# Kernel optimization log

Hardware: AMD Instinct MI355X
Metric: run time of the kernel (lower is better)

The kernel has to match this reference:

```python
import jax, jax.numpy as jnp
import numpy as np

H = 8        # attention heads
TOP_K = 2    # gating top-k
STEPS = 5    # dream_length


def _layernorm(x, w, b, eps=1e-5):
    m = jnp.mean(x, axis=-1, keepdims=True)
    v = jnp.var(x, axis=-1, keepdims=True)
    return (x - m) * jax.lax.rsqrt(v + eps) * w + b


def _mha(x, in_w, in_b, out_w, out_b):
    # torch nn.MultiheadAttention (batch_first, self-attention, eval mode)
    Bx, T, Dm = x.shape
    hd = Dm // H
    qkv = x @ in_w.T + in_b                      # (B, T, 3D)
    q, k, v = jnp.split(qkv, 3, axis=-1)
    sh = lambda t: t.reshape(Bx, T, H, hd).transpose(0, 2, 1, 3)
    q, k, v = sh(q), sh(k), sh(v)
    a = jax.nn.softmax(jnp.einsum('bhqd,bhkd->bhqk', q, k) / np.sqrt(hd).astype(np.float32), axis=-1)
    o = jnp.einsum('bhqk,bhkd->bhqd', a, v).transpose(0, 2, 1, 3).reshape(Bx, T, Dm)
    return o @ out_w.T + out_b


def _triplet_proj(p, x):
    xn = _layernorm(x, p['tln_w'], p['tln_b'])
    h = jax.nn.gelu(xn @ p['tw1'].T + p['tb1'], approximate=False)
    return h @ p['tw2'].T + p['tb2']


def _dream_sequence(p, triplet):
    # triplet: (Bt, 3, D); returns (STEPS, 3, Bt, D)
    Bt, _, Dm = triplet.shape
    seq = [jnp.mean(triplet, axis=1)]
    n_layers = p['an_w'].shape[0]
    for step in range(STEPS):
        st = jnp.stack(seq, axis=1) + p['pos'][:step + 1]   # (Bt, t, D)
        for l in range(n_layers):
            xn = _layernorm(st, p['an_w'][l], p['an_b'][l])
            st = st + _mha(xn, p['in_w'][l], p['in_b'][l], p['ow'][l], p['ob'][l])
            fn = _layernorm(st, p['fn_w'][l], p['fn_b'][l])
            st = st + jax.nn.gelu(fn @ p['w1'][l].T + p['b1'][l], approximate=False) @ p['w2'][l].T + p['b2'][l]
        nxt = _triplet_proj(p, st[:, -1]).reshape(Bt, 3, Dm).mean(axis=1)
        seq.append(nxt)
    embs = jnp.stack(seq[1:], axis=0)                        # (STEPS, Bt, D)
    trip = _triplet_proj(p, embs).reshape(STEPS, Bt, 3, Dm)
    return trip.transpose(0, 2, 1, 3)


def _forward(initial_what, initial_action, initial_result, dream_offsets,
             gw1, gb1, gln_w, gln_b, gw2, gb2,
             pos, an_w, an_b, in_w, in_b, ow, ob, fn_w, fn_b, w1, b1, w2, b2,
             tln_w, tln_b, tw1, tb1, tw2, tb2):
    B, Dm = initial_what.shape
    ND = dream_offsets.shape[0]
    triplet = jnp.stack([initial_what, initial_action, initial_result], axis=1)  # (B, 3, D)
    # --- noisy top-k gating (eval mode: no noise, no dropout) ---
    flat = triplet.reshape(B, 3 * Dm)
    g = jax.nn.gelu(_layernorm(flat @ gw1.T + gb1, gln_w, gln_b), approximate=False)
    logits = g @ gw2.T + gb2                                 # (B, E)
    tv, ti = jax.lax.top_k(logits, TOP_K)
    gates = jax.nn.softmax(tv, axis=-1)
    weights = jnp.zeros_like(logits).at[jnp.arange(B)[:, None], ti].set(gates)
    # --- diversified starts; fold dreams into batch ---
    big = (triplet[None] + dream_offsets[:, None]).reshape(ND * B, 3, Dm)
    ep = dict(pos=pos, an_w=an_w, an_b=an_b, in_w=in_w, in_b=in_b, ow=ow, ob=ob,
              fn_w=fn_w, fn_b=fn_b, w1=w1, b1=b1, w2=w2, b2=b2,
              tln_w=tln_w, tln_b=tln_b, tw1=tw1, tb1=tb1, tw2=tw2, tb2=tb2)
    expert_out = jax.vmap(lambda p: _dream_sequence(p, big))(ep)   # (E, STEPS, 3, ND*B, D)
    E = logits.shape[1]
    expert_out = expert_out.reshape(E, STEPS, 3, ND, B, Dm)
    # weighted combine over experts -> (num_dreams, dream_length, 3, B, D)
    return jnp.einsum('estnbd,be->nstbd', expert_out, weights)


def setup_inputs() -> dict:
    D, E, L, FF, B, ND = 1024, 4, 2, 4096, 512, 3
    ks = iter(jax.random.split(jax.random.key(0), 16))
    nrm = lambda shape, s=1.0: jax.random.normal(next(ks), shape, jnp.float32) * s
    return dict(
        initial_what=nrm((B, D)), initial_action=nrm((B, D)), initial_result=nrm((B, D)),
        dream_offsets=nrm((ND, 3, D), 0.1),
        gw1=nrm((D, 3 * D), (3 * D) ** -0.5), gb1=jnp.zeros((D,)),
        gln_w=jnp.ones((D,)), gln_b=jnp.zeros((D,)),
        gw2=nrm((E, D), D ** -0.5), gb2=jnp.zeros((E,)),
        pos=nrm((E, 10, D)),
        an_w=jnp.ones((E, L, D)), an_b=jnp.zeros((E, L, D)),
        in_w=nrm((E, L, 3 * D, D), D ** -0.5), in_b=jnp.zeros((E, L, 3 * D)),
        ow=nrm((E, L, D, D), D ** -0.5), ob=jnp.zeros((E, L, D)),
        fn_w=jnp.ones((E, L, D)), fn_b=jnp.zeros((E, L, D)),
        w1=nrm((E, L, FF, D), D ** -0.5), b1=jnp.zeros((E, L, FF)),
        w2=nrm((E, L, D, FF), FF ** -0.5), b2=jnp.zeros((E, L, D)),
        tln_w=jnp.ones((E, D)), tln_b=jnp.zeros((E, D)),
        tw1=nrm((E, 2 * D, D), D ** -0.5), tb1=jnp.zeros((E, 2 * D)),
        tw2=nrm((E, 3 * D, 2 * D), (2 * D) ** -0.5), tb2=jnp.zeros((E, 3 * D)),
    )


def reference(initial_what, initial_action, initial_result, dream_offsets,
              gw1, gb1, gln_w, gln_b, gw2, gb2,
              pos, an_w, an_b, in_w, in_b, ow, ob, fn_w, fn_b, w1, b1, w2, b2,
              tln_w, tln_b, tw1, tb1, tw2, tb2):
    return _forward(initial_what, initial_action, initial_result, dream_offsets,
                    gw1, gb1, gln_w, gln_b, gw2, gb2,
                    pos, an_w, an_b, in_w, in_b, ow, ob, fn_w, fn_b, w1, b1, w2, b2,
                    tln_w, tln_b, tw1, tb1, tw2, tb2)
```

## Files before the change

kernel.cpp:

```cpp
#include <hip/hip_runtime.h>
#include <hip/hip_bf16.h>
#include <cstdint>

#define B_  512
#define D_  1024
#define E_  4
#define L_  2
#define FF_ 4096
#define ND_ 3
#define BT_ 1536
#define STEPS_ 5
#define H_ 8
#define PROWS 3584
#define TROWS (PROWS * STEPS_)

typedef __attribute__((ext_vector_type(8))) __bf16 bf16x8;
typedef __attribute__((ext_vector_type(8))) unsigned short u16x8;
typedef __attribute__((ext_vector_type(4))) float f32x4;

static __device__ __forceinline__ float gelu_f(float x) {
    return 0.5f * x * (1.0f + erff(x * 0.70710678118654752f));
}

static __device__ __forceinline__ unsigned short f2bf(float x) {
    unsigned u = __builtin_bit_cast(unsigned, x);
    u = (u + 0x7fff + ((u >> 16) & 1)) >> 16;
    return (unsigned short)u;
}

static __device__ __forceinline__ float bf2f(unsigned short us) {
    unsigned v = (unsigned)us << 16;
    return __builtin_bit_cast(float, v);
}

static __device__ __forceinline__ void gload16(const void* g, void* l) {
    __builtin_amdgcn_global_load_lds(
        (const __attribute__((address_space(1))) unsigned int*)g,
        (__attribute__((address_space(3))) unsigned int*)l, 16, 0, 0);
}

static __device__ __forceinline__ int pad128(int x) { return (x + 127) & ~127; }

template<int ACT, int OUTBF>
__global__ __launch_bounds__(512) void gemm_wf32(
    const unsigned short* __restrict__ A,
    const float* __restrict__ Wb, long wstride, int LDA,
    const float* __restrict__ biasb, long bstride,
    const float* __restrict__ R, long Rld, void* __restrict__ Cout, int N, int K,
    const int* __restrict__ roff, int T)
{
    const long row0 = (long)blockIdx.y * 128;
    if ((int)row0 >= roff[4] * T) return;
    int e = 0;
    while (e < 3 && (int)row0 >= roff[e + 1] * T) ++e;
    const float* W = Wb + (long)e * wstride;
    const float* bias = biasb ? (biasb + (long)e * bstride) : nullptr;

    __shared__ __align__(16) unsigned short As[2 * 128 * 32];
    __shared__ __align__(16) unsigned short Bs[2 * 128 * 32];
    const int t = threadIdx.x;
    const int lane = t & 63;
    const int wid = t >> 6;
    const int wr = wid >> 1;
    const int wc = wid & 1;
    const long col0 = (long)blockIdx.x * 128;
    const int l15 = lane & 15, l4 = lane >> 4;

    f32x4 acc[2][4] = {};

    const unsigned short* Ag = A + (row0 + (t >> 2)) * (long)K + (t & 3) * 8;
    char* AdBase = (char*)As + t * 16;

    const float* Wg = W + (long)(col0 + (t >> 2)) * LDA + (t & 3) * 8;

    const int K32 = K >> 5;
    float4 w0, w1;

    gload16(Ag, AdBase);
    w0 = *(const float4*)(Wg);
    w1 = *(const float4*)(Wg + 4);
    {
        u16x8 p = {f2bf(w0.x), f2bf(w0.y), f2bf(w0.z), f2bf(w0.w),
                   f2bf(w1.x), f2bf(w1.y), f2bf(w1.z), f2bf(w1.w)};
        *(u16x8*)((char*)Bs + t * 16) = p;
    }
    if (K32 > 1) {
        w0 = *(const float4*)(Wg + 32);
        w1 = *(const float4*)(Wg + 36);
    }
    __syncthreads();

    for (int j = 0; j < K32; ++j) {
        const int cur = j & 1;
        const int nxt = cur ^ 1;
        if (j + 1 < K32) {
            gload16(Ag + ((j + 1) << 5), AdBase + nxt * 8192);
            u16x8 p = {f2bf(w0.x), f2bf(w0.y), f2bf(w0.z), f2bf(w0.w),
                       f2bf(w1.x), f2bf(w1.y), f2bf(w1.z), f2bf(w1.w)};
            *(u16x8*)((char*)Bs + nxt * 8192 + t * 16) = p;
        }
        if (j + 2 < K32) {
            const int k2 = (j + 2) << 5;
            w0 = *(const float4*)(Wg + k2);
            w1 = *(const float4*)(Wg + k2 + 4);
        }
        bf16x8 af[2], bf[4];
        #pragma unroll
        for (int m = 0; m < 2; ++m)
            af[m] = *(const bf16x8*)((const char*)As + cur * 8192 + (wr * 32 + m * 16 + l15) * 64 + l4 * 16);
        #pragma unroll
        for (int n = 0; n < 4; ++n)
            bf[n] = *(const bf16x8*)((const char*)Bs + cur * 8192 + (wc * 64 + n * 16 + l15) * 64 + l4 * 16);
        __builtin_amdgcn_s_setprio(1);
        #pragma unroll
        for (int m = 0; m < 2; ++m)
            #pragma unroll
            for (int n = 0; n < 4; ++n)
                acc[m][n] = __builtin_amdgcn_mfma_f32_16x16x32_bf16(af[m], bf[n], acc[m][n], 0, 0, 0);
        __builtin_amdgcn_s_setprio(0);
        __syncthreads();
    }

    #pragma unroll
    for (int n = 0; n < 4; ++n) {
        const long col = col0 + wc * 64 + n * 16 + l15;
        const float bn = bias ? bias[col] : 0.0f;
        #pragma unroll
        for (int m = 0; m < 2; ++m) {
            const long rbase = row0 + wr * 32 + m * 16 + l4 * 4;
            #pragma unroll
            for (int r = 0; r < 4; ++r) {
                float o = acc[m][n][r] + bn;
                if (ACT) o = gelu_f(o);
                const long coff = (rbase + r) * (long)N + col;
                if (R) o += R[(rbase + r) * Rld + col];
                if (OUTBF) ((unsigned short*)Cout)[coff] = f2bf(o);
                else       ((float*)Cout)[coff] = o;
            }
        }
    }
}

__global__ __launch_bounds__(256) void gemm_f32(
    const float* __restrict__ A, const float* __restrict__ W,
    const float* __restrict__ bias, const float* __restrict__ R,
    float* __restrict__ C, int M, int N, int K, int act)
{
    __shared__ float As[16][68];
    __shared__ float Bs[16][68];
    const int tid = threadIdx.x;
    const int tx = tid & 15;
    const int ty = tid >> 4;
    const long row0 = (long)blockIdx.y * 64;
    const long col0 = (long)blockIdx.x * 64;
    const int lr = tid >> 2;
    const int lq = (tid & 3) << 2;
    const float* Ap = A + (row0 + lr) * (long)K + lq;
    const float* Wp = W + (col0 + lr) * (long)K + lq;
    float acc[4][4] = {};
    for (int k0 = 0; k0 < K; k0 += 16) {
        const float4 av = *(const float4*)(Ap + k0);
        const float4 wv = *(const float4*)(Wp + k0);
        __syncthreads();
        As[lq + 0][lr] = av.x; As[lq + 1][lr] = av.y;
        As[lq + 2][lr] = av.z; As[lq + 3][lr] = av.w;
        Bs[lq + 0][lr] = wv.x; Bs[lq + 1][lr] = wv.y;
        Bs[lq + 2][lr] = wv.z; Bs[lq + 3][lr] = wv.w;
        __syncthreads();
        #pragma unroll
        for (int kk = 0; kk < 16; ++kk) {
            const float4 a4 = *(const float4*)&As[kk][ty << 2];
            const float4 b4 = *(const float4*)&Bs[kk][tx << 2];
            const float aa[4] = {a4.x, a4.y, a4.z, a4.w};
            const float bb[4] = {b4.x, b4.y, b4.z, b4.w};
            #pragma unroll
            for (int i = 0; i < 4; ++i)
                #pragma unroll
                for (int j = 0; j < 4; ++j)
                    acc[i][j] = fmaf(aa[i], bb[j], acc[i][j]);
        }
    }
    const float4 bv = *(const float4*)(bias + col0 + (tx << 2));
    const float bb[4] = {bv.x, bv.y, bv.z, bv.w};
    #pragma unroll
    for (int i = 0; i < 4; ++i) {
        const long row = row0 + (ty << 2) + i;
        const long off = row * (long)N + col0 + (tx << 2);
        float o[4];
        #pragma unroll
        for (int j = 0; j < 4; ++j) {
            o[j] = acc[i][j] + bb[j];
            if (act) o[j] = gelu_f(o[j]);
        }
        if (R) {
            const float4 rv = *(const float4*)(R + off);
            o[0] += rv.x; o[1] += rv.y; o[2] += rv.z; o[3] += rv.w;
        }
        *(float4*)(C + off) = make_float4(o[0], o[1], o[2], o[3]);
    }
}

__global__ __launch_bounds__(256) void ln_gate(
    const float* __restrict__ X,
    const float* __restrict__ gamma, const float* __restrict__ beta,
    float* __restrict__ Y)
{
    const long r = blockIdx.x;
    const int tid = threadIdx.x;
    __shared__ float red[8];
    const float4 v = *(const float4*)(X + (r << 10) + (tid << 2));
    float s = v.x + v.y + v.z + v.w;
    #pragma unroll
    for (int off = 32; off; off >>= 1) s += __shfl_xor(s, off);
    if ((tid & 63) == 0) red[tid >> 6] = s;
    __syncthreads();
    const float mean = (red[0] + red[1] + red[2] + red[3]) * (1.0f / 1024.0f);
    const float dx = v.x - mean, dy = v.y - mean, dz = v.z - mean, dw = v.w - mean;
    float s2 = dx * dx + dy * dy + dz * dz + dw * dw;
    #pragma unroll
    for (int off = 32; off; off >>= 1) s2 += __shfl_xor(s2, off);
    if ((tid & 63) == 0) red[4 + (tid >> 6)] = s2;
    __syncthreads();
    const float var = (red[4] + red[5] + red[6] + red[7]) * (1.0f / 1024.0f);
    const float inv = rsqrtf(var + 1e-5f);
    const float4 g = *(const float4*)(gamma + (tid << 2));
    const float4 b = *(const float4*)(beta + (tid << 2));
    float o0 = gelu_f(dx * inv * g.x + b.x);
    float o1 = gelu_f(dy * inv * g.y + b.y);
    float o2 = gelu_f(dz * inv * g.z + b.z);
    float o3 = gelu_f(dw * inv * g.w + b.w);
    *(float4*)(Y + (r << 10) + (tid << 2)) = make_float4(o0, o1, o2, o3);
}

__global__ __launch_bounds__(256) void ln_bt(
    const float* __restrict__ X, long xstride,
    const float* __restrict__ gammaB, const float* __restrict__ betaB, long gstride,
    unsigned short* __restrict__ Y, const int* __restrict__ roff, int T)
{
    const long r = blockIdx.x;
    if ((int)r >= roff[4] * T) return;
    int e = 0;
    while (e < 3 && (int)r >= roff[e + 1] * T) ++e;
    const float* gamma = gammaB + (long)e * gstride;
    const float* beta  = betaB  + (long)e * gstride;

    const int tid = threadIdx.x;
    __shared__ float red[8];
    const float4 v = *(const float4*)(X + r * xstride + (tid << 2));
    float s = v.x + v.y + v.z + v.w;
    #pragma unroll
    for (int off = 32; off; off >>= 1) s += __shfl_xor(s, off);
    if ((tid & 63) == 0) red[tid >> 6] = s;
    __syncthreads();
    const float mean = (red[0] + red[1] + red[2] + red[3]) * (1.0f / 1024.0f);
    const float dx = v.x - mean, dy = v.y - mean, dz = v.z - mean, dw = v.w - mean;
    float s2 = dx * dx + dy * dy + dz * dz + dw * dw;
    #pragma unroll
    for (int off = 32; off; off >>= 1) s2 += __shfl_xor(s2, off);
    if ((tid & 63) == 0) red[4 + (tid >> 6)] = s2;
    __syncthreads();
    const float var = (red[4] + red[5] + red[6] + red[7]) * (1.0f / 1024.0f);
    const float inv = rsqrtf(var + 1e-5f);
    const float4 g = *(const float4*)(gamma + (tid << 2));
    const float4 b = *(const float4*)(beta + (tid << 2));
    const float o0 = dx * inv * g.x + b.x;
    const float o1 = dy * inv * g.y + b.y;
    const float o2 = dz * inv * g.z + b.z;
    const float o3 = dw * inv * g.w + b.w;
    ushort4 o = make_ushort4(f2bf(o0), f2bf(o1), f2bf(o2), f2bf(o3));
    *(ushort4*)(Y + (r << 10) + (tid << 2)) = o;
}

__global__ __launch_bounds__(256) void ln_st_bt(
    const float* __restrict__ seq, const float* __restrict__ posb,
    float* __restrict__ st,
    const float* __restrict__ gammaB, const float* __restrict__ betaB, long gstride,
    unsigned short* __restrict__ Y, const int* __restrict__ roff, int T)
{
    const int r = blockIdx.x;
    const int prow = r / T;
    if (prow >= roff[4]) return;
    int e = 0;
    while (e < 3 && prow >= roff[e + 1]) ++e;
    const int tau = r - prow * T;
    const float* gamma = gammaB + (long)e * gstride;
    const float* beta  = betaB  + (long)e * gstride;

    const int tid = threadIdx.x;
    const int d4 = tid << 2;
    __shared__ float red[8];
    const float4 sv = *(const float4*)(seq + (((long)tau * PROWS + prow) << 10) + d4);
    const float4 pv = *(const float4*)(posb + (((long)e * 10 + tau) << 10) + d4);
    const float4 v = make_float4(sv.x + pv.x, sv.y + pv.y, sv.z + pv.z, sv.w + pv.w);
    *(float4*)(st + ((long)r << 10) + d4) = v;

    float s = v.x + v.y + v.z + v.w;
    #pragma unroll
    for (int off = 32; off; off >>= 1) s += __shfl_xor(s, off);
    if ((tid & 63) == 0) red[tid >> 6] = s;
    __syncthreads();
    const float mean = (red[0] + red[1] + red[2] + red[3]) * (1.0f / 1024.0f);
    const float dx = v.x - mean, dy = v.y - mean, dz = v.z - mean, dw = v.w - mean;
    float s2 = dx * dx + dy * dy + dz * dz + dw * dw;
    #pragma unroll
    for (int off = 32; off; off >>= 1) s2 += __shfl_xor(s2, off);
    if ((tid & 63) == 0) red[4 + (tid >> 6)] = s2;
    __syncthreads();
    const float var = (red[4] + red[5] + red[6] + red[7]) * (1.0f / 1024.0f);
    const float inv = rsqrtf(var + 1e-5f);
    const float4 g = *(const float4*)(gamma + d4);
    const float4 b = *(const float4*)(beta + d4);
    const float o0 = dx * inv * g.x + b.x;
    const float o1 = dy * inv * g.y + b.y;
    const float o2 = dz * inv * g.z + b.z;
    const float o3 = dw * inv * g.w + b.w;
    ushort4 o = make_ushort4(f2bf(o0), f2bf(o1), f2bf(o2), f2bf(o3));
    *(ushort4*)(Y + ((long)r << 10) + d4) = o;
}

template<int TT>
__global__ __launch_bounds__(256) void attn_bt(
    const unsigned short* __restrict__ qkv, unsigned short* __restrict__ o,
    const int* __restrict__ roff)
{
    const int item = (int)(((long)blockIdx.x * 256 + threadIdx.x) >> 6);
    const int lane = threadIdx.x & 63;
    const int tq = item % TT;
    const int h  = (item / TT) & 7;
    const int i  = item / (TT * 8);
    if (i >= roff[4]) return;
    const unsigned short* base = qkv + (long)i * TT * 3072;
    const unsigned short* q = base + (long)tq * 3072 + h * 128;
    const float q0 = bf2f(q[lane]), q1 = bf2f(q[lane + 64]);
    float s[TT];
    const float scale = 0.088388347648318447f;
    #pragma unroll
    for (int tk = 0; tk < TT; ++tk) {
        const unsigned short* k = base + (long)tk * 3072 + 1024 + h * 128;
        float p = q0 * bf2f(k[lane]) + q1 * bf2f(k[lane + 64]);
        #pragma unroll
        for (int off = 32; off; off >>= 1) p += __shfl_xor(p, off);
        s[tk] = p * scale;
    }
    float m = s[0];
    #pragma unroll
    for (int tk = 1; tk < TT; ++tk) m = fmaxf(m, s[tk]);
    float den = 0.f;
    #pragma unroll
    for (int tk = 0; tk < TT; ++tk) { s[tk] = expf(s[tk] - m); den += s[tk]; }
    float o0 = 0.f, o1 = 0.f;
    #pragma unroll
    for (int tk = 0; tk < TT; ++tk) {
        const unsigned short* v = base + (long)tk * 3072 + 2048 + h * 128;
        o0 += s[tk] * bf2f(v[lane]); o1 += s[tk] * bf2f(v[lane + 64]);
    }
    const float id = 1.0f / den;
    unsigned short* op = o + ((long)i * TT + tq) * 1024 + h * 128;
    op[lane] = f2bf(o0 * id); op[lane + 64] = f2bf(o1 * id);
}

template<int TT>
__global__ __launch_bounds__(256) void attn_last(
    const unsigned short* __restrict__ qkv, unsigned short* __restrict__ o,
    const int* __restrict__ roff)
{
    const int item = (int)(((long)blockIdx.x * 256 + threadIdx.x) >> 6);
    const int lane = threadIdx.x & 63;
    const int h  = item & 7;
    const int i  = item >> 3;
    if (i >= roff[4]) return;
    const unsigned short* base = qkv + (long)i * TT * 3072;
    const unsigned short* q = base + (long)(TT - 1) * 3072 + h * 128;
    const float q0 = bf2f(q[lane]), q1 = bf2f(q[lane + 64]);
    float s[TT];
    const float scale = 0.088388347648318447f;
    #pragma unroll
    for (int tk = 0; tk < TT; ++tk) {
        const unsigned short* k = base + (long)tk * 3072 + 1024 + h * 128;
        float p = q0 * bf2f(k[lane]) + q1 * bf2f(k[lane + 64]);
        #pragma unroll
        for (int off = 32; off; off >>= 1) p += __shfl_xor(p, off);
        s[tk] = p * scale;
    }
    float m = s[0];
    #pragma unroll
    for (int tk = 1; tk < TT; ++tk) m = fmaxf(m, s[tk]);
    float den = 0.f;
    #pragma unroll
    for (int tk = 0; tk < TT; ++tk) { s[tk] = expf(s[tk] - m); den += s[tk]; }
    float o0 = 0.f, o1 = 0.f;
    #pragma unroll
    for (int tk = 0; tk < TT; ++tk) {
        const unsigned short* v = base + (long)tk * 3072 + 2048 + h * 128;
        o0 += s[tk] * bf2f(v[lane]); o1 += s[tk] * bf2f(v[lane + 64]);
    }
    const float id = 1.0f / den;
    unsigned short* op = o + (long)i * 1024 + h * 128;
    op[lane] = f2bf(o0 * id); op[lane + 64] = f2bf(o1 * id);
}

__global__ __launch_bounds__(256) void gate_kernel(
    const float* __restrict__ g, const float* __restrict__ gw2,
    const float* __restrict__ gb2, float* __restrict__ wout)
{
    const int b = (int)(((long)blockIdx.x * 256 + threadIdx.x) >> 6);
    const int lane = threadIdx.x & 63;
    float acc[E_] = {};
    const float* row = g + (long)b * 1024;
    for (int d = lane; d < 1024; d += 64) {
        const float x = row[d];
        #pragma unroll
        for (int j = 0; j < E_; ++j) acc[j] += x * gw2[j * 1024 + d];
    }
    #pragma unroll
    for (int j = 0; j < E_; ++j) {
        #pragma unroll
        for (int off = 32; off; off >>= 1) acc[j] += __shfl_xor(acc[j], off);
        acc[j] += gb2[j];
    }
    int i0 = 0; float v0 = acc[0];
    #pragma unroll
    for (int j = 1; j < E_; ++j) if (acc[j] > v0) { v0 = acc[j]; i0 = j; }
    int i1 = -1; float v1 = -1e30f;
    #pragma unroll
    for (int j = 0; j < E_; ++j) if (j != i0 && acc[j] > v1) { v1 = acc[j]; i1 = j; }
    const float p1 = expf(v1 - v0);
    const float den = 1.0f + p1;
    const float g0 = 1.0f / den, g1 = p1 / den;
    if (lane < E_) wout[b * E_ + lane] = (lane == i0) ? g0 : (lane == i1) ? g1 : 0.0f;
}

__global__ __launch_bounds__(64) void build_idx2_kernel(
    const float* __restrict__ wbuf, int* __restrict__ idx,
    int* __restrict__ cnt3, int* __restrict__ roff)
{
    const int lane = threadIdx.x;
    int pads[E_];
    for (int e = 0; e < E_; ++e) {
        int* my = idx + e * BT_;
        int base = 0;
        for (int chunk = 0; chunk < 8; ++chunk) {
            const int b = chunk * 64 + lane;
            const bool sel = wbuf[b * E_ + e] > 0.0f;
            const unsigned long long mask = __ballot(sel);
            const int pos = base + (int)__popcll(mask & ((1ull << lane) - 1ull));
            if (sel) {
                my[3 * pos + 0] = b;
                my[3 * pos + 1] = 512 + b;
                my[3 * pos + 2] = 1024 + b;
            }
            base += (int)__popcll(mask);
        }
        if (lane == 0) cnt3[e] = 3 * base;
        pads[e] = pad128(3 * base);
    }
    if (lane == 0) {
        roff[0] = 0;
        for (int e = 0; e < E_; ++e) roff[e + 1] = roff[e] + pads[e];
    }
}

__global__ __launch_bounds__(256) void seq0_bt(
    const float* __restrict__ w, const float* __restrict__ a,
    const float* __restrict__ rr, const float* __restrict__ doff,
    const int* __restrict__ idx, const int* __restrict__ cnt3,
    const int* __restrict__ roff, float* __restrict__ seq0)
{
    const int prow = blockIdx.x;
    if (prow >= roff[4]) return;
    int e = 0;
    while (e < 3 && prow >= roff[e + 1]) ++e;
    const int j = prow - roff[e];
    const int d4 = threadIdx.x << 2;
    float4 res = make_float4(0.f, 0.f, 0.f, 0.f);
    if (j < cnt3[e]) {
        const int v = idx[e * BT_ + j];
        const int n = v >> 9, b = v & 511;
        const float4 x = *(const float4*)(w + ((long)b << 10) + d4);
        const float4 y = *(const float4*)(a + ((long)b << 10) + d4);
        const float4 z = *(const float4*)(rr + ((long)b << 10) + d4);
        const float4 o0 = *(const float4*)(doff + ((long)(n * 3 + 0) << 10) + d4);
        const float4 o1 = *(const float4*)(doff + ((long)(n * 3 + 1) << 10) + d4);
        const float4 o2 = *(const float4*)(doff + ((long)(n * 3 + 2) << 10) + d4);
        const float c = 1.0f / 3.0f;
        res = make_float4(
            (x.x + y.x + z.x + o0.x + o1.x + o2.x) * c,
            (x.y + y.y + z.y + o0.y + o1.y + o2.y) * c,
            (x.z + y.z + z.z + o0.z + o1.z + o2.z) * c,
            (x.w + y.w + z.w + o0.w + o1.w + o2.w) * c);
    }
    *(float4*)(seq0 + ((long)prow << 10) + d4) = res;
}

__global__ __launch_bounds__(256) void mean3_bt(
    const float* __restrict__ O, float* __restrict__ dst,
    const int* __restrict__ roff)
{
    const int r = blockIdx.x;
    if (r >= roff[4]) return;
    const int d4 = threadIdx.x << 2;
    const float* p = O + (long)r * 3072 + d4;
    const float4 x = *(const float4*)p;
    const float4 y = *(const float4*)(p + 1024);
    const float4 z = *(const float4*)(p + 2048);
    const float c = 1.0f / 3.0f;
    *(float4*)(dst + ((long)r << 10) + d4) = make_float4(
        (x.x + y.x + z.x) * c, (x.y + y.y + z.y) * c,
        (x.z + y.z + z.z) * c, (x.w + y.w + z.w) * c);
}

__global__ __launch_bounds__(256) void scatter_bt(
    const float* __restrict__ O, const float* __restrict__ wbuf,
    const int* __restrict__ idx, const int* __restrict__ cnt3,
    const int* __restrict__ roff, float* __restrict__ out, int e, int s)
{
    const int r = blockIdx.x;
    if (r >= cnt3[e]) return;
    const int prow = roff[e] + r;
    const int v = idx[e * BT_ + r];
    const int n = v >> 9, b = v & 511;
    const float wgt = wbuf[b * E_ + e];
    const int d4 = threadIdx.x << 2;
    const float* orow = O + (long)prow * 3072;
    #pragma unroll
    for (int c = 0; c < 3; ++c) {
        const float4 t = *(const float4*)(orow + c * 1024 + d4);
        float* op = out + (((long)((n * STEPS_ + s) * 3 + c) * B_ + b) << 10) + d4;
        float4 o = *(const float4*)op;
        o.x += wgt * t.x; o.y += wgt * t.y; o.z += wgt * t.z; o.w += wgt * t.w;
        *(float4*)op = o;
    }
}

__global__ __launch_bounds__(256) void build_flat_kernel(
    const float* __restrict__ w, const float* __restrict__ a,
    const float* __restrict__ r, float* __restrict__ flat)
{
    const long e4 = ((long)blockIdx.x * 256 + threadIdx.x) << 2;
    const int b = (int)(e4 / 3072);
    const int cd = (int)(e4 % 3072);
    const int c = cd >> 10, d = cd & 1023;
    const float* src = (c == 0) ? w : (c == 1) ? a : r;
    *(float4*)(flat + e4) = *(const float4*)(src + ((long)b << 10) + d);
}

__global__ __launch_bounds__(256) void zero_kernel(float* __restrict__ p, long n4)
{
    const long stride = (long)gridDim.x * 256;
    for (long i = (long)blockIdx.x * 256 + threadIdx.x; i < n4; i += stride)
        *(float4*)(p + i * 4) = make_float4(0.f, 0.f, 0.f, 0.f);
}


extern "C" void kernel_launch(void* const* d_in, const int* in_sizes, int n_in,
                              void* d_out, int out_size, void* d_ws, size_t ws_size,
                              hipStream_t stream)
{
    const float* iw   = (const float*)d_in[0];
    const float* ia   = (const float*)d_in[1];
    const float* ir   = (const float*)d_in[2];
    const float* doff = (const float*)d_in[3];
    const float* gw1  = (const float*)d_in[4];
    const float* gb1  = (const float*)d_in[5];
    const float* glnw = (const float*)d_in[6];
    const float* glnb = (const float*)d_in[7];
    const float* gw2  = (const float*)d_in[8];
    const float* gb2  = (const float*)d_in[9];
    const float* pos  = (const float*)d_in[10];
    const float* anw  = (const float*)d_in[11];
    const float* anb  = (const float*)d_in[12];
    const float* inw  = (const float*)d_in[13];
    const float* inb  = (const float*)d_in[14];
    const float* oww  = (const float*)d_in[15];
    const float* owb  = (const float*)d_in[16];
    const float* fnw  = (const float*)d_in[17];
    const float* fnb  = (const float*)d_in[18];
    const float* w1   = (const float*)d_in[19];
    const float* b1   = (const float*)d_in[20];
    const float* w2   = (const float*)d_in[21];
    const float* b2   = (const float*)d_in[22];
    const float* tlnw = (const float*)d_in[23];
    const float* tlnb = (const float*)d_in[24];
    const float* tw1  = (const float*)d_in[25];
    const float* tb1  = (const float*)d_in[26];
    const float* tw2  = (const float*)d_in[27];
    const float* tb2  = (const float*)d_in[28];
    float* out = (float*)d_out;

    float* ws    = (float*)d_ws;
    float* wbuf  = ws;
    int*   cnt3  = (int*)(wbuf + 2048);
    int*   roff  = cnt3 + 16;
    int*   idxb  = roff + 16;
    float* flatb = (float*)(idxb + 4 * BT_);
    float* glin  = flatb + (long)B_ * 3072;
    float* seq   = glin + (long)B_ * 1024;
    float* st    = seq + 6L * PROWS * 1024;
    unsigned short* xnB  = (unsigned short*)(st + (long)TROWS * 1024);
    unsigned short* bigB = xnB + (long)TROWS * 1024;
    unsigned short* Fbuf = bigB;
    unsigned short* axB  = xnB;
    float* Obuf = (float*)(bigB + 16777216);
    float* stL  = seq + 5L * PROWS * 1024;
    if (ws_size < 79175712UL * sizeof(float)) return;

    build_flat_kernel<<<B_ * 3, 256, 0, stream>>>(iw, ia, ir, flatb);
    gemm_f32<<<dim3(16, 8), 256, 0, stream>>>(flatb, gw1, gb1, nullptr, glin, B_, 1024, 3072, 0);
    ln_gate<<<B_, 256, 0, stream>>>(glin, glnw, glnb, glin);
    gate_kernel<<<B_ / 4, 256, 0, stream>>>(glin, gw2, gb2, wbuf);
    build_idx2_kernel<<<1, 64, 0, stream>>>(wbuf, idxb, cnt3, roff);

    zero_kernel<<<2048, 256, 0, stream>>>(out, (long)ND_ * STEPS_ * 3 * B_ * 1024 / 4);

    seq0_bt<<<PROWS, 256, 0, stream>>>(iw, ia, ir, doff, idxb, cnt3, roff, seq);

    for (int t = 0; t < STEPS_; ++t) {
        const int T = t + 1;
        const int MT = PROWS * T;

        {
            const int l = 0;
            ln_st_bt<<<MT, 256, 0, stream>>>(seq, pos, st,
                                             anw + l * 1024, anb + l * 1024,
                                             (long)L_ * 1024, xnB, roff, T);
            gemm_wf32<0, 1><<<dim3(24, MT / 128), 512, 0, stream>>>(
                xnB, inw + (long)l * 3072 * 1024, (long)L_ * 3072 * 1024, 1024,
                inb + l * 3072, (long)L_ * 3072, nullptr, 0, bigB, 3072, 1024, roff, T);
            switch (T) {
                case 1: attn_bt<1><<<PROWS * 8 * 1 / 4, 256, 0, stream>>>(bigB, xnB, roff); break;
                case 2: attn_bt<2><<<PROWS * 8 * 2 / 4, 256, 0, stream>>>(bigB, xnB, roff); break;
                case 3: attn_bt<3><<<PROWS * 8 * 3 / 4, 256, 0, stream>>>(bigB, xnB, roff); break;
                case 4: attn_bt<4><<<PROWS * 8 * 4 / 4, 256, 0, stream>>>(bigB, xnB, roff); break;
                case 5: attn_bt<5><<<PROWS * 8 * 5 / 4, 256, 0, stream>>>(bigB, xnB, roff); break;
            }
            gemm_wf32<0, 0><<<dim3(8, MT / 128), 512, 0, stream>>>(
                xnB, oww + (long)l * 1024 * 1024, (long)L_ * 1024 * 1024, 1024,
                owb + l * 1024, (long)L_ * 1024, st, 1024, st, 1024, 1024, roff, T);
            ln_bt<<<MT, 256, 0, stream>>>(st, 1024, fnw + l * 1024, fnb + l * 1024,
                                          (long)L_ * 1024, xnB, roff, T);
            for (int c = 0; c < 2; ++c) {
                gemm_wf32<1, 1><<<dim3(16, MT / 128), 512, 0, stream>>>(
                    xnB, w1 + (long)l * 4096 * 1024 + (long)c * 2048 * 1024,
                    (long)L_ * 4096 * 1024, 1024,
                    b1 + l * 4096 + c * 2048, (long)L_ * 4096, nullptr, 0, bigB, 2048, 1024, roff, T);
                gemm_wf32<0, 0><<<dim3(8, MT / 128), 512, 0, stream>>>(
                    bigB, w2 + (long)l * 1024 * 4096 + (long)c * 2048,
                    (long)L_ * 1024 * 4096, 4096,
                    (c == 0) ? (b2 + l * 1024) : nullptr, (long)L_ * 1024,
                    st, 1024, st, 1024, 2048, roff, T);
            }
        }

        {
            const int l = 1;
            ln_bt<<<MT, 256, 0, stream>>>(st, 1024, anw + l * 1024, anb + l * 1024,
                                          (long)L_ * 1024, xnB, roff, T);
            gemm_wf32<0, 1><<<dim3(24, MT / 128), 512, 0, stream>>>(
                xnB, inw + (long)l * 3072 * 1024, (long)L_ * 3072 * 1024, 1024,
                inb + l * 3072, (long)L_ * 3072, nullptr, 0, bigB, 3072, 1024, roff, T);
            switch (T) {
                case 1: attn_last<1><<<PROWS * 8 / 4, 256, 0, stream>>>(bigB, axB, roff); break;
                case 2: attn_last<2><<<PROWS * 8 / 4, 256, 0, stream>>>(bigB, axB, roff); break;
                case 3: attn_last<3><<<PROWS * 8 / 4, 256, 0, stream>>>(bigB, axB, roff); break;
                case 4: attn_last<4><<<PROWS * 8 / 4, 256, 0, stream>>>(bigB, axB, roff); break;
                case 5: attn_last<5><<<PROWS * 8 / 4, 256, 0, stream>>>(bigB, axB, roff); break;
            }
            gemm_wf32<0, 0><<<dim3(8, PROWS / 128), 512, 0, stream>>>(
                axB, oww + (long)l * 1024 * 1024, (long)L_ * 1024 * 1024, 1024,
                owb + l * 1024, (long)L_ * 1024,
                st + (long)t * 1024, (long)T * 1024, stL, 1024, 1024, roff, 1);
            ln_bt<<<PROWS, 256, 0, stream>>>(stL, 1024, fnw + l * 1024, fnb + l * 1024,
                                             (long)L_ * 1024, xnB, roff, 1);
            for (int c = 0; c < 2; ++c) {
                gemm_wf32<1, 1><<<dim3(16, PROWS / 128), 512, 0, stream>>>(
                    xnB, w1 + (long)l * 4096 * 1024 + (long)c * 2048 * 1024,
                    (long)L_ * 4096 * 1024, 1024,
                    b1 + l * 4096 + c * 2048, (long)L_ * 4096, nullptr, 0, Fbuf, 2048, 1024, roff, 1);
                gemm_wf32<0, 0><<<dim3(8, PROWS / 128), 512, 0, stream>>>(
                    Fbuf, w2 + (long)l * 1024 * 4096 + (long)c * 2048,
                    (long)L_ * 1024 * 4096, 4096,
                    (c == 0) ? (b2 + l * 1024) : nullptr, (long)L_ * 1024,
                    stL, 1024, stL, 1024, 2048, roff, 1);
            }
        }

        ln_bt<<<PROWS, 256, 0, stream>>>(stL, 1024, tlnw, tlnb, 1024, xnB, roff, 1);
        gemm_wf32<1, 1><<<dim3(16, PROWS / 128), 512, 0, stream>>>(
            xnB, tw1, 2048L * 1024, 1024, tb1, 2048, nullptr, 0, Fbuf, 2048, 1024, roff, 1);
        gemm_wf32<0, 0><<<dim3(24, PROWS / 128), 512, 0, stream>>>(
            Fbuf, tw2, 3072L * 2048, 2048, tb2, 3072, nullptr, 0, Obuf, 3072, 2048, roff, 1);
        mean3_bt<<<PROWS, 256, 0, stream>>>(Obuf, seq + (long)(t + 1) * PROWS * 1024, roff);
    }
    for (int s = 0; s < STEPS_; ++s) {
        ln_bt<<<PROWS, 256, 0, stream>>>(seq + (long)(s + 1) * PROWS * 1024, 1024,
                                         tlnw, tlnb, 1024, xnB, roff, 1);
        gemm_wf32<1, 1><<<dim3(16, PROWS / 128), 512, 0, stream>>>(
            xnB, tw1, 2048L * 1024, 1024, tb1, 2048, nullptr, 0, Fbuf, 2048, 1024, roff, 1);
        gemm_wf32<0, 0><<<dim3(24, PROWS / 128), 512, 0, stream>>>(
            Fbuf, tw2, 3072L * 2048, 2048, tb2, 3072, nullptr, 0, Obuf, 3072, 2048, roff, 1);
        for (int e = 0; e < E_; ++e)
            scatter_bt<<<BT_, 256, 0, stream>>>(Obuf, wbuf, idxb, cnt3, roff, out, e, s);
    }
}
```

Baseline: 6.909 ms.

## Pre-convert weights to bf16 once and use bf16-weight GEMM kernel

Adds a pass that converts all expert weight matrices from f32 to bf16 into an extra workspace region. A new GEMM kernel then loads both operands as bf16 via direct-to-LDS loads, replacing per-tile f32 loads and register conversion. This halves weight bandwidth and removes conversion ALU work in every GEMM. In exchange it costs an upfront conversion pass each call and needs a larger workspace; if the workspace is too small it falls back to the old kernel.

```diff
diff --git a/kernel.cpp b/kernel.cpp
--- a/kernel.cpp
+++ b/kernel.cpp
@@ -70,7 +70,6 @@
 
     const unsigned short* Ag = A + (row0 + (t >> 2)) * (long)K + (t & 3) * 8;
     char* AdBase = (char*)As + t * 16;
-
     const float* Wg = W + (long)(col0 + (t >> 2)) * LDA + (t & 3) * 8;
 
     const int K32 = K >> 5;
@@ -103,6 +102,89 @@
             const int k2 = (j + 2) << 5;
             w0 = *(const float4*)(Wg + k2);
             w1 = *(const float4*)(Wg + k2 + 4);
+        }
+        bf16x8 af[2], bf[4];
+        #pragma unroll
+        for (int m = 0; m < 2; ++m)
+            af[m] = *(const bf16x8*)((const char*)As + cur * 8192 + (wr * 32 + m * 16 + l15) * 64 + l4 * 16);
+        #pragma unroll
+        for (int n = 0; n < 4; ++n)
+            bf[n] = *(const bf16x8*)((const char*)Bs + cur * 8192 + (wc * 64 + n * 16 + l15) * 64 + l4 * 16);
+        __builtin_amdgcn_s_setprio(1);
+        #pragma unroll
+        for (int m = 0; m < 2; ++m)
+            #pragma unroll
+            for (int n = 0; n < 4; ++n)
+                acc[m][n] = __builtin_amdgcn_mfma_f32_16x16x32_bf16(af[m], bf[n], acc[m][n], 0, 0, 0);
+        __builtin_amdgcn_s_setprio(0);
+        __syncthreads();
+    }
+
+    #pragma unroll
+    for (int n = 0; n < 4; ++n) {
+        const long col = col0 + wc * 64 + n * 16 + l15;
+        const float bn = bias ? bias[col] : 0.0f;
+        #pragma unroll
+        for (int m = 0; m < 2; ++m) {
+            const long rbase = row0 + wr * 32 + m * 16 + l4 * 4;
+            #pragma unroll
+            for (int r = 0; r < 4; ++r) {
+                float o = acc[m][n][r] + bn;
+                if (ACT) o = gelu_f(o);
+                const long coff = (rbase + r) * (long)N + col;
+                if (R) o += R[(rbase + r) * Rld + col];
+                if (OUTBF) ((unsigned short*)Cout)[coff] = f2bf(o);
+                else       ((float*)Cout)[coff] = o;
+            }
+        }
+    }
+}
+
+template<int ACT, int OUTBF>
+__global__ __launch_bounds__(512) void gemm_bb(
+    const unsigned short* __restrict__ A,
+    const unsigned short* __restrict__ Wb, long wstride, int LDA,
+    const float* __restrict__ biasb, long bstride,
+    const float* __restrict__ R, long Rld, void* __restrict__ Cout, int N, int K,
+    const int* __restrict__ roff, int T)
+{
+    const long row0 = (long)blockIdx.y * 128;
+    if ((int)row0 >= roff[4] * T) return;
+    int e = 0;
+    while (e < 3 && (int)row0 >= roff[e + 1] * T) ++e;
+    const unsigned short* W = Wb + (long)e * wstride;
+    const float* bias = biasb ? (biasb + (long)e * bstride) : nullptr;
+
+    __shared__ __align__(16) unsigned short As[2 * 128 * 32];
+    __shared__ __align__(16) unsigned short Bs[2 * 128 * 32];
+    const int t = threadIdx.x;
+    const int lane = t & 63;
+    const int wid = t >> 6;
+    const int wr = wid >> 1;
+    const int wc = wid & 1;
+    const long col0 = (long)blockIdx.x * 128;
+    const int l15 = lane & 15, l4 = lane >> 4;
+
+    f32x4 acc[2][4] = {};
+
+    const unsigned short* Ag = A + (row0 + (t >> 2)) * (long)K + (t & 3) * 8;
+    const unsigned short* Wg = W + (long)(col0 + (t >> 2)) * LDA + (t & 3) * 8;
+    char* AdBase = (char*)As + t * 16;
+    char* BdBase = (char*)Bs + t * 16;
+
+    const int K32 = K >> 5;
+
+    gload16(Ag, AdBase);
+    gload16(Wg, BdBase);
+    __syncthreads();
+
+    for (int j = 0; j < K32; ++j) {
+        const int cur = j & 1;
+        const int nxt = cur ^ 1;
+        if (j + 1 < K32) {
+            const int k1 = (j + 1) << 5;
+            gload16(Ag + k1, AdBase + nxt * 8192);
+            gload16(Wg + k1, BdBase + nxt * 8192);
         }
         bf16x8 af[2], bf[4];
         #pragma unroll
@@ -549,6 +631,29 @@
     const long stride = (long)gridDim.x * 256;
     for (long i = (long)blockIdx.x * 256 + threadIdx.x; i < n4; i += stride)
         *(float4*)(p + i * 4) = make_float4(0.f, 0.f, 0.f, 0.f);
+}
+
+__global__ __launch_bounds__(256) void cvt_bf16_kernel(
+    const float* __restrict__ src, unsigned short* __restrict__ dst, long n4)
+{
+    const long stride = (long)gridDim.x * 256;
+    for (long i = (long)blockIdx.x * 256 + threadIdx.x; i < n4; i += stride) {
+        const float4 v = *(const float4*)(src + i * 4);
+        ushort4 o = make_ushort4(f2bf(v.x), f2bf(v.y), f2bf(v.z), f2bf(v.w));
+        *(ushort4*)(dst + i * 4) = o;
+    }
+}
+
+template<int ACT, int OUTBF>
+static inline void G(bool mir, dim3 grid, hipStream_t s,
+                     const unsigned short* A,
+                     const float* Wf, const unsigned short* Wm, long wstride, int LDA,
+                     const float* bias, long bstride,
+                     const float* R, long Rld, void* C, int N, int K,
+                     const int* roff, int T)
+{
+    if (mir) gemm_bb<ACT, OUTBF><<<grid, 512, 0, s>>>(A, Wm, wstride, LDA, bias, bstride, R, Rld, C, N, K, roff, T);
+    else     gemm_wf32<ACT, OUTBF><<<grid, 512, 0, s>>>(A, Wf, wstride, LDA, bias, bstride, R, Rld, C, N, K, roff, T);
 }
 
 
@@ -604,6 +709,15 @@
     float* stL  = seq + 5L * PROWS * 1024;
     if (ws_size < 79175712UL * sizeof(float)) return;
 
+    const bool mir = (ws_size >= 146284576UL * sizeof(float));
+    unsigned short* wM   = (unsigned short*)(ws + 79175712UL);
+    unsigned short* winM = wM;
+    unsigned short* wowM = winM + (long)E_ * L_ * 3072 * 1024;
+    unsigned short* w1M  = wowM + (long)E_ * L_ * 1024 * 1024;
+    unsigned short* w2M  = w1M  + (long)E_ * L_ * 4096 * 1024;
+    unsigned short* t1M  = w2M  + (long)E_ * L_ * 1024 * 4096;
+    unsigned short* t2M  = t1M  + (long)E_ * 2048 * 1024;
+
     build_flat_kernel<<<B_ * 3, 256, 0, stream>>>(iw, ia, ir, flatb);
     gemm_f32<<<dim3(16, 8), 256, 0, stream>>>(flatb, gw1, gb1, nullptr, glin, B_, 1024, 3072, 0);
     ln_gate<<<B_, 256, 0, stream>>>(glin, glnw, glnb, glin);
@@ -612,6 +726,15 @@
 
     zero_kernel<<<2048, 256, 0, stream>>>(out, (long)ND_ * STEPS_ * 3 * B_ * 1024 / 4);
 
+    if (mir) {
+        cvt_bf16_kernel<<<2048, 256, 0, stream>>>(inw, winM, (long)E_ * L_ * 3072 * 1024 / 4);
+        cvt_bf16_kernel<<<2048, 256, 0, stream>>>(oww, wowM, (long)E_ * L_ * 1024 * 1024 / 4);
+        cvt_bf16_kernel<<<2048, 256, 0, stream>>>(w1,  w1M,  (long)E_ * L_ * 4096 * 1024 / 4);
+        cvt_bf16_kernel<<<2048, 256, 0, stream>>>(w2,  w2M,  (long)E_ * L_ * 1024 * 4096 / 4);
+        cvt_bf16_kernel<<<2048, 256, 0, stream>>>(tw1, t1M,  (long)E_ * 2048 * 1024 / 4);
+        cvt_bf16_kernel<<<2048, 256, 0, stream>>>(tw2, t2M,  (long)E_ * 3072 * 2048 / 4);
+    }
+
     seq0_bt<<<PROWS, 256, 0, stream>>>(iw, ia, ir, doff, idxb, cnt3, roff, seq);
 
     for (int t = 0; t < STEPS_; ++t) {
@@ -623,9 +746,10 @@
             ln_st_bt<<<MT, 256, 0, stream>>>(seq, pos, st,
                                              anw + l * 1024, anb + l * 1024,
                                              (long)L_ * 1024, xnB, roff, T);
-            gemm_wf32<0, 1><<<dim3(24, MT / 128), 512, 0, stream>>>(
-                xnB, inw + (long)l * 3072 * 1024, (long)L_ * 3072 * 1024, 1024,
-                inb + l * 3072, (long)L_ * 3072, nullptr, 0, bigB, 3072, 1024, roff, T);
+            G<0, 1>(mir, dim3(24, MT / 128), stream, xnB,
+                    inw + (long)l * 3072 * 1024, winM + (long)l * 3072 * 1024,
+                    (long)L_ * 3072 * 1024, 1024,
+                    inb + l * 3072, (long)L_ * 3072, nullptr, 0, bigB, 3072, 1024, roff, T);
             switch (T) {
                 case 1: attn_bt<1><<<PROWS * 8 * 1 / 4, 256, 0, stream>>>(bigB, xnB, roff); break;
                 case 2: attn_bt<2><<<PROWS * 8 * 2 / 4, 256, 0, stream>>>(bigB, xnB, roff); break;
@@ -633,21 +757,24 @@
                 case 4: attn_bt<4><<<PROWS * 8 * 4 / 4, 256, 0, stream>>>(bigB, xnB, roff); break;
                 case 5: attn_bt<5><<<PROWS * 8 * 5 / 4, 256, 0, stream>>>(bigB, xnB, roff); break;
             }
-            gemm_wf32<0, 0><<<dim3(8, MT / 128), 512, 0, stream>>>(
-                xnB, oww + (long)l * 1024 * 1024, (long)L_ * 1024 * 1024, 1024,
-                owb + l * 1024, (long)L_ * 1024, st, 1024, st, 1024, 1024, roff, T);
+            G<0, 0>(mir, dim3(8, MT / 128), stream, xnB,
+                    oww + (long)l * 1024 * 1024, wowM + (long)l * 1024 * 1024,
+                    (long)L_ * 1024 * 1024, 1024,
+                    owb + l * 1024, (long)L_ * 1024, st, 1024, st, 1024, 1024, roff, T);
             ln_bt<<<MT, 256, 0, stream>>>(st, 1024, fnw + l * 1024, fnb + l * 1024,
                                           (long)L_ * 1024, xnB, roff, T);
             for (int c = 0; c < 2; ++c) {
-                gemm_wf32<1, 1><<<dim3(16, MT / 128), 512, 0, stream>>>(
-                    xnB, w1 + (long)l * 4096 * 1024 + (long)c * 2048 * 1024,
-                    (long)L_ * 4096 * 1024, 1024,
-                    b1 + l * 4096 + c * 2048, (long)L_ * 4096, nullptr, 0, bigB, 2048, 1024, roff, T);
-                gemm_wf32<0, 0><<<dim3(8, MT / 128), 512, 0, stream>>>(
-                    bigB, w2 + (long)l * 1024 * 4096 + (long)c * 2048,
-                    (long)L_ * 1024 * 4096, 4096,
-                    (c == 0) ? (b2 + l * 1024) : nullptr, (long)L_ * 1024,
-                    st, 1024, st, 1024, 2048, roff, T);
+                G<1, 1>(mir, dim3(16, MT / 128), stream, xnB,
+                        w1 + (long)l * 4096 * 1024 + (long)c * 2048 * 1024,
+                        w1M + (long)l * 4096 * 1024 + (long)c * 2048 * 1024,
+                        (long)L_ * 4096 * 1024, 1024,
+                        b1 + l * 4096 + c * 2048, (long)L_ * 4096, nullptr, 0, bigB, 2048, 1024, roff, T);
+                G<0, 0>(mir, dim3(8, MT / 128), stream, bigB,
+                        w2 + (long)l * 1024 * 4096 + (long)c * 2048,
+                        w2M + (long)l * 1024 * 4096 + (long)c * 2048,
+                        (long)L_ * 1024 * 4096, 4096,
+                        (c == 0) ? (b2 + l * 1024) : nullptr, (long)L_ * 1024,
+                        st, 1024, st, 1024, 2048, roff, T);
             }
         }
 
@@ -655,9 +782,10 @@
             const int l = 1;
             ln_bt<<<MT, 256, 0, stream>>>(st, 1024, anw + l * 1024, anb + l * 1024,
                                           (long)L_ * 1024, xnB, roff, T);
-            gemm_wf32<0, 1><<<dim3(24, MT / 128), 512, 0, stream>>>(
-                xnB, inw + (long)l * 3072 * 1024, (long)L_ * 3072 * 1024, 1024,
-                inb + l * 3072, (long)L_ * 3072, nullptr, 0, bigB, 3072, 1024, roff, T);
+            G<0, 1>(mir, dim3(24, MT / 128), stream, xnB,
+                    inw + (long)l * 3072 * 1024, winM + (long)l * 3072 * 1024,
+                    (long)L_ * 3072 * 1024, 1024,
+                    inb + l * 3072, (long)L_ * 3072, nullptr, 0, bigB, 3072, 1024, roff, T);
             switch (T) {
                 case 1: attn_last<1><<<PROWS * 8 / 4, 256, 0, stream>>>(bigB, axB, roff); break;
                 case 2: attn_last<2><<<PROWS * 8 / 4, 256, 0, stream>>>(bigB, axB, roff); break;
@@ -665,39 +793,42 @@
                 case 4: attn_last<4><<<PROWS * 8 / 4, 256, 0, stream>>>(bigB, axB, roff); break;
                 case 5: attn_last<5><<<PROWS * 8 / 4, 256, 0, stream>>>(bigB, axB, roff); break;
             }
-            gemm_wf32<0, 0><<<dim3(8, PROWS / 128), 512, 0, stream>>>(
-                axB, oww + (long)l * 1024 * 1024, (long)L_ * 1024 * 1024, 1024,
-                owb + l * 1024, (long)L_ * 1024,
-                st + (long)t * 1024, (long)T * 1024, stL, 1024, 1024, roff, 1);
+            G<0, 0>(mir, dim3(8, PROWS / 128), stream, axB,
+                    oww + (long)l * 1024 * 1024, wowM + (long)l * 1024 * 1024,
+                    (long)L_ * 1024 * 1024, 1024,
+                    owb + l * 1024, (long)L_ * 1024,
+                    st + (long)t * 1024, (long)T * 1024, stL, 1024, 1024, roff, 1);
             ln_bt<<<PROWS, 256, 0, stream>>>(stL, 1024, fnw + l * 1024, fnb + l * 1024,
                                              (long)L_ * 1024, xnB, roff, 1);
             for (int c = 0; c < 2; ++c) {
-                gemm_wf32<1, 1><<<dim3(16, PROWS / 128), 512, 0, stream>>>(
-                    xnB, w1 + (long)l * 4096 * 1024 + (long)c * 2048 * 1024,
-                    (long)L_ * 4096 * 1024, 1024,
-                    b1 + l * 4096 + c * 2048, (long)L_ * 4096, nullptr, 0, Fbuf, 2048, 1024, roff, 1);
-                gemm_wf32<0, 0><<<dim3(8, PROWS / 128), 512, 0, stream>>>(
-                    Fbuf, w2 + (long)l * 1024 * 4096 + (long)c * 2048,
-                    (long)L_ * 1024 * 4096, 4096,
-                    (c == 0) ? (b2 + l * 1024) : nullptr, (long)L_ * 1024,
-                    stL, 1024, stL, 1024, 2048, roff, 1);
+                G<1, 1>(mir, dim3(16, PROWS / 128), stream, xnB,
+                        w1 + (long)l * 4096 * 1024 + (long)c * 2048 * 1024,
+                        w1M + (long)l * 4096 * 1024 + (long)c * 2048 * 1024,
+                        (long)L_ * 4096 * 1024, 1024,
+                        b1 + l * 4096 + c * 2048, (long)L_ * 4096, nullptr, 0, Fbuf, 2048, 1024, roff, 1);
+                G<0, 0>(mir, dim3(8, PROWS / 128), stream, Fbuf,
+                        w2 + (long)l * 1024 * 4096 + (long)c * 2048,
+                        w2M + (long)l * 1024 * 4096 + (long)c * 2048,
+                        (long)L_ * 1024 * 4096, 4096,
+                        (c == 0) ? (b2 + l * 1024) : nullptr, (long)L_ * 1024,
+                        stL, 1024, stL, 1024, 2048, roff, 1);
             }
         }
 
         ln_bt<<<PROWS, 256, 0, stream>>>(stL, 1024, tlnw, tlnb, 1024, xnB, roff, 1);
-        gemm_wf32<1, 1><<<dim3(16, PROWS / 128), 512, 0, stream>>>(
-            xnB, tw1, 2048L * 1024, 1024, tb1, 2048, nullptr, 0, Fbuf, 2048, 1024, roff, 1);
-        gemm_wf32<0, 0><<<dim3(24, PROWS / 128), 512, 0, stream>>>(
-            Fbuf, tw2, 3072L * 2048, 2048, tb2, 3072, nullptr, 0, Obuf, 3072, 2048, roff, 1);
+        G<1, 1>(mir, dim3(16, PROWS / 128), stream, xnB,
+                tw1, t1M, 2048L * 1024, 1024, tb1, 2048, nullptr, 0, Fbuf, 2048, 1024, roff, 1);
+        G<0, 0>(mir, dim3(24, PROWS / 128), stream, Fbuf,
+                tw2, t2M, 3072L * 2048, 2048, tb2, 3072, nullptr, 0, Obuf, 3072, 2048, roff, 1);
         mean3_bt<<<PROWS, 256, 0, stream>>>(Obuf, seq + (long)(t + 1) * PROWS * 1024, roff);
     }
     for (int s = 0; s < STEPS_; ++s) {
         ln_bt<<<PROWS, 256, 0, stream>>>(seq + (long)(s + 1) * PROWS * 1024, 1024,
                                          tlnw, tlnb, 1024, xnB, roff, 1);
-        gemm_wf32<1, 1><<<dim3(16, PROWS / 128), 512, 0, stream>>>(
-            xnB, tw1, 2048L * 1024, 1024, tb1, 2048, nullptr, 0, Fbuf, 2048, 1024, roff, 1);
-        gemm_wf32<0, 0><<<dim3(24, PROWS / 128), 512, 0, stream>>>(
-            Fbuf, tw2, 3072L * 2048, 2048, tb2, 3072, nullptr, 0, Obuf, 3072, 2048, roff, 1);
+        G<1, 1>(mir, dim3(16, PROWS / 128), stream, xnB,
+                tw1, t1M, 2048L * 1024, 1024, tb1, 2048, nullptr, 0, Fbuf, 2048, 1024, roff, 1);
+        G<0, 0>(mir, dim3(24, PROWS / 128), stream, Fbuf,
+                tw2, t2M, 3072L * 2048, 2048, tb2, 3072, nullptr, 0, Obuf, 3072, 2048, roff, 1);
         for (int e = 0; e < E_; ++e)
             scatter_bt<<<BT_, 256, 0, stream>>>(Obuf, wbuf, idxb, cnt3, roff, out, e, s);
     }
```

New measurement: 6.935 ms. About the same (+0.4%).
